# Optimization experiments

Measured on AMD Instinct MI355X. Metric: run time of the kernel, lower is better.

## Reference

```python
import jax, jax.numpy as jnp
import numpy as np

N_SPANS = 4096
EMB_DIM = 384
HEADS = 4
DECAY_LAMBDA = 5.0
THRESHOLD = 0.1
NEG_SLOPE = 0.2  # PyG GATConv default leaky_relu slope


def setup_inputs() -> dict:
    key = jax.random.key(0)
    k1, k2, k3, k4, k5, k6 = jax.random.split(key, 6)
    embeddings = jax.random.normal(k1, (N_SPANS, EMB_DIM), dtype=jnp.float32)
    span_positions = jnp.sort(
        jax.random.randint(k2, (N_SPANS, 2), 0, 100000), axis=1
    ).astype(jnp.int64)
    # GATConv params: lin (no bias), per-head attention vectors, output bias
    glorot = 1.0 / np.sqrt(EMB_DIM)
    W = jax.random.normal(k3, (EMB_DIM, HEADS, EMB_DIM), dtype=jnp.float32) * glorot
    att_src = jax.random.normal(k4, (HEADS, EMB_DIM), dtype=jnp.float32) * glorot
    att_dst = jax.random.normal(k5, (HEADS, EMB_DIM), dtype=jnp.float32) * glorot
    bias = jnp.zeros((EMB_DIM,), dtype=jnp.float32)
    return {
        "embeddings": embeddings,
        "span_positions": span_positions,
        "W": W,
        "att_src": att_src,
        "att_dst": att_dst,
        "bias": bias,
    }


def _adjacency_mask(embeddings):
    # A_ij = cos_sim(e_i, e_j) * exp(-|i - j| / lambda); edges where A > 0.1
    n = embeddings.shape[0]
    en = embeddings / jnp.linalg.norm(embeddings, axis=1, keepdims=True)
    cos_sim = en @ en.T  # [N, N]
    idx = jnp.arange(n, dtype=embeddings.dtype)
    decay = jnp.exp(-jnp.abs(idx[None, :] - idx[:, None]) / DECAY_LAMBDA)
    adj = cos_sim * decay
    # diagonal is 1.0 > threshold, so self-loops (required by GATConv) are present
    return adj > THRESHOLD  # symmetric mask: mask[i, j] == edge j -> i


def reference(embeddings, span_positions, W, att_src, att_dst, bias):
    mask = _adjacency_mask(embeddings)  # [N_dst, N_src]
    # GATConv(heads=4, concat=False): project, per-head additive attention
    x = jnp.einsum("nd,dhe->nhe", embeddings, W)  # [N, H, E]
    a_src = jnp.einsum("nhe,he->nh", x, att_src)  # [N, H]
    a_dst = jnp.einsum("nhe,he->nh", x, att_dst)  # [N, H]
    # logits[i, j, h] for edge j -> i
    logits = jax.nn.leaky_relu(a_dst[:, None, :] + a_src[None, :, :], NEG_SLOPE)
    logits = jnp.where(mask[:, :, None], logits, jnp.float32(-jnp.inf))
    alpha = jax.nn.softmax(logits, axis=1)  # softmax over incoming sources j
    out = jnp.einsum("ijh,jhe->ihe", alpha, x)  # [N, H, E]
    out = out.mean(axis=1) + bias  # concat=False -> mean over heads, then bias
    return out
```

## Files before the change

### kernel.cpp

```cpp
#include <hip/hip_runtime.h>
#include <hip/hip_bf16.h>
#include <math.h>

#define N_SPANS 4096
#define EMB 384
#define HEADS 4
#define HE (HEADS * EMB)
#define BAND 11
#define BW (2 * BAND + 1)

typedef short bf16x8 __attribute__((ext_vector_type(8)));
typedef float f32x4 __attribute__((ext_vector_type(4)));
typedef unsigned short u16x8 __attribute__((ext_vector_type(8)));

__device__ __forceinline__ unsigned short f2bf(float f) {
    union { float f; unsigned u; } x; x.f = f;
    unsigned r = x.u + 0x7fffu + ((x.u >> 16) & 1u);
    return (unsigned short)(r >> 16);
}

__device__ __forceinline__ float wave_sum(float v) {
    #pragma unroll
    for (int off = 32; off; off >>= 1) v += __shfl_xor(v, off, 64);
    return v;
}
__device__ __forceinline__ float wave_max(float v) {
    #pragma unroll
    for (int off = 32; off; off >>= 1) v = fmaxf(v, __shfl_xor(v, off, 64));
    return v;
}

__global__ __launch_bounds__(256) void row_norms(const float* __restrict__ E,
                                                 float* __restrict__ invn) {
    int n = blockIdx.x * 4 + (threadIdx.x >> 6);
    int lane = threadIdx.x & 63;
    const float* er = E + n * EMB;
    float s = 0.f;
    #pragma unroll
    for (int m = 0; m < 6; ++m) { float v = er[m * 64 + lane]; s += v * v; }
    s = wave_sum(s);
    if (lane == 0) invn[n] = 1.0f / sqrtf(s);
}

__global__ __launch_bounds__(256) void transpose_w(const float* __restrict__ W,
                                                   unsigned short* __restrict__ Wt) {
    __shared__ float t[32][33];
    int n0 = blockIdx.x * 32;
    int k0 = blockIdx.y * 32;
    int tx = threadIdx.x & 31, ty = threadIdx.x >> 5;
    #pragma unroll
    for (int q = 0; q < 4; ++q)
        t[ty + q * 8][tx] = W[(k0 + ty + q * 8) * HE + n0 + tx];
    __syncthreads();
    #pragma unroll
    for (int q = 0; q < 4; ++q)
        Wt[(n0 + ty + q * 8) * EMB + k0 + tx] = f2bf(t[tx][ty + q * 8]);
}

__global__ __launch_bounds__(256) void gemm_proj(const float* __restrict__ E,
                                                 const unsigned short* __restrict__ Wt,
                                                 float* __restrict__ X) {
    __shared__ unsigned short As[128 * 32];
    __shared__ unsigned short Bs[128 * 32];
    const int tid = threadIdx.x;
    const int lane = tid & 63;
    const int wave = tid >> 6;
    const int m0 = blockIdx.y * 128;
    const int n0 = blockIdx.x * 128;
    const int wr = (wave >> 1) * 64;
    const int wc = (wave & 1) * 64;
    const int quad = lane >> 4;
    const int l16 = lane & 15;

    f32x4 acc[4][4];
    #pragma unroll
    for (int i = 0; i < 4; ++i)
        #pragma unroll
        for (int j = 0; j < 4; ++j) acc[i][j] = 0.f;

    for (int kt = 0; kt < 12; ++kt) {
        __syncthreads();
        #pragma unroll
        for (int c = 0; c < 4; ++c) {
            int ch = tid + c * 256;
            int row = ch >> 3, cc = ch & 7;
            const float4 v = *(const float4*)(E + (m0 + row) * EMB + kt * 32 + cc * 4);
            ushort4 b;
            b.x = f2bf(v.x); b.y = f2bf(v.y); b.z = f2bf(v.z); b.w = f2bf(v.w);
            *(ushort4*)(&As[row * 32 + cc * 4]) = b;
        }
        #pragma unroll
        for (int c = 0; c < 2; ++c) {
            int ch = tid + c * 256;
            int row = ch >> 2, cc = ch & 3;
            *(u16x8*)(&Bs[row * 32 + cc * 8]) =
                *(const u16x8*)(Wt + (n0 + row) * EMB + kt * 32 + cc * 8);
        }
        __syncthreads();

        bf16x8 af[4], bfr[4];
        #pragma unroll
        for (int t = 0; t < 4; ++t) {
            af[t]  = *(const bf16x8*)(&As[(wr + t * 16 + l16) * 32 + quad * 8]);
            bfr[t] = *(const bf16x8*)(&Bs[(wc + t * 16 + l16) * 32 + quad * 8]);
        }
        #pragma unroll
        for (int ti = 0; ti < 4; ++ti)
            #pragma unroll
            for (int tj = 0; tj < 4; ++tj)
                acc[ti][tj] = __builtin_amdgcn_mfma_f32_16x16x32_bf16(
                    af[ti], bfr[tj], acc[ti][tj], 0, 0, 0);
    }
    #pragma unroll
    for (int ti = 0; ti < 4; ++ti)
        #pragma unroll
        for (int tj = 0; tj < 4; ++tj) {
            int col = n0 + wc + tj * 16 + l16;
            #pragma unroll
            for (int r = 0; r < 4; ++r) {
                int row = m0 + wr + ti * 16 + quad * 4 + r;
                X[row * HE + col] = acc[ti][tj][r];
            }
        }
}

__global__ __launch_bounds__(256) void att_vecs(const float* __restrict__ X,
                                                const float* __restrict__ att_src,
                                                const float* __restrict__ att_dst,
                                                float* __restrict__ asrc,
                                                float* __restrict__ adst) {
    int n = blockIdx.x;
    int lane = threadIdx.x & 63, h = threadIdx.x >> 6;
    const float* xr = X + n * HE + h * EMB;
    float ss = 0.f, sd = 0.f;
    #pragma unroll
    for (int m = 0; m < 6; ++m) {
        int e = m * 64 + lane;
        float v = xr[e];
        ss += v * att_src[h * EMB + e];
        sd += v * att_dst[h * EMB + e];
    }
    ss = wave_sum(ss);
    sd = wave_sum(sd);
    if (lane == 0) { asrc[n * HEADS + h] = ss; adst[n * HEADS + h] = sd; }
}

__global__ __launch_bounds__(256) void band_attn(const float* __restrict__ E,
                                                 const float* __restrict__ invn,
                                                 const float* __restrict__ asrc,
                                                 const float* __restrict__ adst,
                                                 const float* __restrict__ X,
                                                 const float* __restrict__ bias,
                                                 float* __restrict__ out) {
    const int i = blockIdx.x;
    const int tid = threadIdx.x;
    const int lane = tid & 63, wave = tid >> 6;

    __shared__ float ei[EMB];
    __shared__ float alpha_s[HEADS][BW];
    __shared__ int maskv[BW];
    __shared__ int list[BW];
    __shared__ int cnt;

    for (int d = tid; d < EMB; d += 256) ei[d] = E[i * EMB + d];
    __syncthreads();

    const float inv_i = invn[i];
    for (int it = 0; it < 6; ++it) {
        int jo = it * 4 + wave;
        if (jo < BW) {
            int j = i - BAND + jo;
            bool valid = (j >= 0) && (j < N_SPANS);
            float s = 0.f;
            if (valid) {
                const float* ej = E + j * EMB;
                #pragma unroll
                for (int m = 0; m < 6; ++m) {
                    int d = m * 64 + lane;
                    s += ei[d] * ej[d];
                }
                s = wave_sum(s);
            }
            if (lane == 0) {
                int mflag = 0;
                if (valid) {
                    float cosv = s * inv_i * invn[j];
                    int dd = jo - BAND; if (dd < 0) dd = -dd;
                    float a = cosv * expf(-(float)dd * 0.2f);
                    if (a > 0.1f) mflag = 1;
                }
                maskv[jo] = mflag;
            }
        }
    }
    __syncthreads();

    {
        const int h = wave;
        const int jo = lane;
        float logit = -INFINITY;
        if (jo < BW && maskv[jo]) {
            int j = i - BAND + jo;
            float z = adst[i * HEADS + h] + asrc[j * HEADS + h];
            logit = (z >= 0.f) ? z : 0.2f * z;
        }
        float mx = wave_max(logit);
        float ex = (jo < BW) ? expf(logit - mx) : 0.f;
        float sm = wave_sum(ex);
        if (jo < BW) alpha_s[h][jo] = ex / sm;
    }
    __syncthreads();

    if (tid == 0) {
        int c = 0;
        for (int jo = 0; jo < BW; ++jo) if (maskv[jo]) list[c++] = jo;
        cnt = c;
    }
    __syncthreads();

    const int c = cnt;
    for (int e = tid; e < EMB; e += 256) {
        float acc = 0.f;
        for (int ii = 0; ii < c; ++ii) {
            int jo = list[ii];
            int j = i - BAND + jo;
            const float* xb = X + j * HE + e;
            #pragma unroll
            for (int h = 0; h < HEADS; ++h)
                acc += alpha_s[h][jo] * xb[h * EMB];
        }
        out[i * EMB + e] = 0.25f * acc + bias[e];
    }
}

extern "C" void kernel_launch(void* const* d_in, const int* in_sizes, int n_in,
                              void* d_out, int out_size, void* d_ws, size_t ws_size,
                              hipStream_t stream) {
    const float* E       = (const float*)d_in[0];
    const float* W       = (const float*)d_in[2];
    const float* att_src = (const float*)d_in[3];
    const float* att_dst = (const float*)d_in[4];
    const float* bias    = (const float*)d_in[5];
    float* out = (float*)d_out;

    char* ws = (char*)d_ws;
    float* X            = (float*)ws;
    unsigned short* Wt  = (unsigned short*)(ws + 25165824);
    float* invn         = (float*)(ws + 25165824 + 1179648);
    float* asrc         = invn + 4096;
    float* adst         = asrc + 4096 * HEADS;

    row_norms<<<1024, 256, 0, stream>>>(E, invn);
    transpose_w<<<dim3(48, 12), 256, 0, stream>>>(W, Wt);
    gemm_proj<<<dim3(12, 32), 256, 0, stream>>>(E, Wt, X);
    att_vecs<<<4096, 256, 0, stream>>>(X, att_src, att_dst, asrc, adst);
    band_attn<<<4096, 256, 0, stream>>>(E, invn, asrc, adst, X, bias, out);
}
```

Measured before the change: 120.6 us.

## Fuse prep kernels, attention-vector reduction into GEMM epilogue, store projection in bf16

Merges row norms, the weight transpose, a pre-pass casting embeddings to bf16, and zeroing of the atomic accumulators into one prep launch. The GEMM now loads tiles with direct global-to-LDS loads and computes the per-head source/destination attention scalars in its epilogue via shuffles and atomics, which removes the separate att_vecs pass over X. X is stored as bf16, halving its write and the band_attn gather traffic. The cost is extra bf16 rounding on X, atomic ordering nondeterminism in the attention scalars, and fewer kernel launches.

Measured after the change: 119.0 us (median of 2 runs). Within noise of the previous version (-1.3%).

```diff
diff --git a/kernel.cpp b/kernel.cpp
--- a/kernel.cpp
+++ b/kernel.cpp
@@ -11,13 +11,15 @@
 
 typedef short bf16x8 __attribute__((ext_vector_type(8)));
 typedef float f32x4 __attribute__((ext_vector_type(4)));
-typedef unsigned short u16x8 __attribute__((ext_vector_type(8)));
 
 __device__ __forceinline__ unsigned short f2bf(float f) {
     union { float f; unsigned u; } x; x.f = f;
     unsigned r = x.u + 0x7fffu + ((x.u >> 16) & 1u);
     return (unsigned short)(r >> 16);
 }
+__device__ __forceinline__ float bf2f(unsigned short u) {
+    union { unsigned u; float f; } x; x.u = ((unsigned)u) << 16; return x.f;
+}
 
 __device__ __forceinline__ float wave_sum(float v) {
     #pragma unroll
@@ -30,36 +32,67 @@
     return v;
 }
 
-__global__ __launch_bounds__(256) void row_norms(const float* __restrict__ E,
-                                                 float* __restrict__ invn) {
-    int n = blockIdx.x * 4 + (threadIdx.x >> 6);
-    int lane = threadIdx.x & 63;
-    const float* er = E + n * EMB;
-    float s = 0.f;
-    #pragma unroll
-    for (int m = 0; m < 6; ++m) { float v = er[m * 64 + lane]; s += v * v; }
-    s = wave_sum(s);
-    if (lane == 0) invn[n] = 1.0f / sqrtf(s);
-}
-
-__global__ __launch_bounds__(256) void transpose_w(const float* __restrict__ W,
-                                                   unsigned short* __restrict__ Wt) {
-    __shared__ float t[32][33];
-    int n0 = blockIdx.x * 32;
-    int k0 = blockIdx.y * 32;
-    int tx = threadIdx.x & 31, ty = threadIdx.x >> 5;
-    #pragma unroll
-    for (int q = 0; q < 4; ++q)
-        t[ty + q * 8][tx] = W[(k0 + ty + q * 8) * HE + n0 + tx];
-    __syncthreads();
-    #pragma unroll
-    for (int q = 0; q < 4; ++q)
-        Wt[(n0 + ty + q * 8) * EMB + k0 + tx] = f2bf(t[tx][ty + q * 8]);
-}
-
-__global__ __launch_bounds__(256) void gemm_proj(const float* __restrict__ E,
+__device__ __forceinline__ void gl2lds16(const void* g, void* l) {
+    __builtin_amdgcn_global_load_lds(
+        (const __attribute__((address_space(1))) void*)(uintptr_t)g,
+        (__attribute__((address_space(3))) void*)(unsigned)(uintptr_t)l,
+        16, 0, 0);
+}
+
+__global__ __launch_bounds__(256) void prep(const float* __restrict__ E,
+                                            const float* __restrict__ W,
+                                            unsigned short* __restrict__ Ebf,
+                                            unsigned short* __restrict__ Wt,
+                                            float* __restrict__ invn,
+                                            float* __restrict__ attacc) {
+    __shared__ float tile[32][33];
+    const int b = blockIdx.x;
+    const int tid = threadIdx.x;
+    if (b < 1024) {
+        const int lane = tid & 63, w = tid >> 6;
+        const int n = b * 4 + w;
+        const float4* er = (const float4*)(E + n * EMB);
+        unsigned short* orow = Ebf + n * EMB;
+        float s = 0.f;
+        float4 v0 = er[lane];
+        s += v0.x * v0.x + v0.y * v0.y + v0.z * v0.z + v0.w * v0.w;
+        ushort4 c0;
+        c0.x = f2bf(v0.x); c0.y = f2bf(v0.y); c0.z = f2bf(v0.z); c0.w = f2bf(v0.w);
+        ((ushort4*)orow)[lane] = c0;
+        if (lane < 32) {
+            float4 v1 = er[lane + 64];
+            s += v1.x * v1.x + v1.y * v1.y + v1.z * v1.z + v1.w * v1.w;
+            ushort4 c1;
+            c1.x = f2bf(v1.x); c1.y = f2bf(v1.y); c1.z = f2bf(v1.z); c1.w = f2bf(v1.w);
+            ((ushort4*)orow)[lane + 64] = c1;
+        }
+        s = wave_sum(s);
+        if (lane == 0) invn[n] = 1.0f / sqrtf(s);
+    } else if (b < 1600) {
+        const int t = b - 1024;
+        const int n0 = (t % 48) * 32;
+        const int k0 = (t / 48) * 32;
+        const int tx = tid & 31, ty = tid >> 5;
+        #pragma unroll
+        for (int q = 0; q < 4; ++q)
+            tile[ty + q * 8][tx] = W[(k0 + ty + q * 8) * HE + n0 + tx];
+        __syncthreads();
+        #pragma unroll
+        for (int q = 0; q < 4; ++q)
+            Wt[(n0 + ty + q * 8) * EMB + k0 + tx] = f2bf(tile[tx][ty + q * 8]);
+    } else {
+        const int t = b - 1600;
+        ((float4*)attacc)[t * 256 + tid] = make_float4(0.f, 0.f, 0.f, 0.f);
+    }
+}
+
+__global__ __launch_bounds__(256) void gemm_attn(const unsigned short* __restrict__ Ebf,
                                                  const unsigned short* __restrict__ Wt,
-                                                 float* __restrict__ X) {
+                                                 const float* __restrict__ attS,
+                                                 const float* __restrict__ attD,
+                                                 unsigned short* __restrict__ Xb,
+                                                 float* __restrict__ asrc,
+                                                 float* __restrict__ adst) {
     __shared__ unsigned short As[128 * 32];
     __shared__ unsigned short Bs[128 * 32];
     const int tid = threadIdx.x;
@@ -72,6 +105,11 @@
     const int quad = lane >> 4;
     const int l16 = lane & 15;
 
+    const char* Ab = (const char*)Ebf + (size_t)(m0 + wave * 32 + (lane >> 2)) * 768 + (lane & 3) * 16;
+    const char* Bb = (const char*)Wt  + (size_t)(n0 + wave * 32 + (lane >> 2)) * 768 + (lane & 3) * 16;
+    char* AsB = (char*)As + wave * 32 * 64;
+    char* BsB = (char*)Bs + wave * 32 * 64;
+
     f32x4 acc[4][4];
     #pragma unroll
     for (int i = 0; i < 4; ++i)
@@ -79,23 +117,12 @@
         for (int j = 0; j < 4; ++j) acc[i][j] = 0.f;
 
     for (int kt = 0; kt < 12; ++kt) {
+        const int kb = kt * 64;
         __syncthreads();
-        #pragma unroll
-        for (int c = 0; c < 4; ++c) {
-            int ch = tid + c * 256;
-            int row = ch >> 3, cc = ch & 7;
-            const float4 v = *(const float4*)(E + (m0 + row) * EMB + kt * 32 + cc * 4);
-            ushort4 b;
-            b.x = f2bf(v.x); b.y = f2bf(v.y); b.z = f2bf(v.z); b.w = f2bf(v.w);
-            *(ushort4*)(&As[row * 32 + cc * 4]) = b;
-        }
-        #pragma unroll
-        for (int c = 0; c < 2; ++c) {
-            int ch = tid + c * 256;
-            int row = ch >> 2, cc = ch & 3;
-            *(u16x8*)(&Bs[row * 32 + cc * 8]) =
-                *(const u16x8*)(Wt + (n0 + row) * EMB + kt * 32 + cc * 8);
-        }
+        gl2lds16(Ab + kb,            AsB);
+        gl2lds16(Ab + kb + 16 * 768, AsB + 16 * 64);
+        gl2lds16(Bb + kb,            BsB);
+        gl2lds16(Bb + kb + 16 * 768, BsB + 16 * 64);
         __syncthreads();
 
         bf16x8 af[4], bfr[4];
@@ -111,6 +138,38 @@
                 acc[ti][tj] = __builtin_amdgcn_mfma_f32_16x16x32_bf16(
                     af[ti], bfr[tj], acc[ti][tj], 0, 0, 0);
     }
+
+    const int hblk = (n0 + wc) / EMB;
+    float aS[4], aD[4];
+    #pragma unroll
+    for (int tj = 0; tj < 4; ++tj) {
+        int col = n0 + wc + tj * 16 + l16;
+        aS[tj] = attS[col];
+        aD[tj] = attD[col];
+    }
+    #pragma unroll
+    for (int ti = 0; ti < 4; ++ti)
+        #pragma unroll
+        for (int r = 0; r < 4; ++r) {
+            float ps = 0.f, pd = 0.f;
+            #pragma unroll
+            for (int tj = 0; tj < 4; ++tj) {
+                float v = acc[ti][tj][r];
+                ps += v * aS[tj];
+                pd += v * aD[tj];
+            }
+            #pragma unroll
+            for (int off = 1; off < 16; off <<= 1) {
+                ps += __shfl_xor(ps, off, 64);
+                pd += __shfl_xor(pd, off, 64);
+            }
+            if (l16 == 0) {
+                int row = m0 + wr + ti * 16 + quad * 4 + r;
+                atomicAdd(&asrc[row * HEADS + hblk], ps);
+                atomicAdd(&adst[row * HEADS + hblk], pd);
+            }
+        }
+
     #pragma unroll
     for (int ti = 0; ti < 4; ++ti)
         #pragma unroll
@@ -119,37 +178,16 @@
             #pragma unroll
             for (int r = 0; r < 4; ++r) {
                 int row = m0 + wr + ti * 16 + quad * 4 + r;
-                X[row * HE + col] = acc[ti][tj][r];
-            }
-        }
-}
-
-__global__ __launch_bounds__(256) void att_vecs(const float* __restrict__ X,
-                                                const float* __restrict__ att_src,
-                                                const float* __restrict__ att_dst,
-                                                float* __restrict__ asrc,
-                                                float* __restrict__ adst) {
-    int n = blockIdx.x;
-    int lane = threadIdx.x & 63, h = threadIdx.x >> 6;
-    const float* xr = X + n * HE + h * EMB;
-    float ss = 0.f, sd = 0.f;
-    #pragma unroll
-    for (int m = 0; m < 6; ++m) {
-        int e = m * 64 + lane;
-        float v = xr[e];
-        ss += v * att_src[h * EMB + e];
-        sd += v * att_dst[h * EMB + e];
-    }
-    ss = wave_sum(ss);
-    sd = wave_sum(sd);
-    if (lane == 0) { asrc[n * HEADS + h] = ss; adst[n * HEADS + h] = sd; }
+                Xb[row * HE + col] = f2bf(acc[ti][tj][r]);
+            }
+        }
 }
 
 __global__ __launch_bounds__(256) void band_attn(const float* __restrict__ E,
                                                  const float* __restrict__ invn,
                                                  const float* __restrict__ asrc,
                                                  const float* __restrict__ adst,
-                                                 const float* __restrict__ X,
+                                                 const unsigned short* __restrict__ Xb,
                                                  const float* __restrict__ bias,
                                                  float* __restrict__ out) {
     const int i = blockIdx.x;
@@ -224,10 +262,10 @@
         for (int ii = 0; ii < c; ++ii) {
             int jo = list[ii];
             int j = i - BAND + jo;
-            const float* xb = X + j * HE + e;
+            const unsigned short* xb = Xb + j * HE + e;
             #pragma unroll
             for (int h = 0; h < HEADS; ++h)
-                acc += alpha_s[h][jo] * xb[h * EMB];
+                acc += alpha_s[h][jo] * bf2f(xb[h * EMB]);
         }
         out[i * EMB + e] = 0.25f * acc + bias[e];
     }
@@ -244,15 +282,14 @@
     float* out = (float*)d_out;
 
     char* ws = (char*)d_ws;
-    float* X            = (float*)ws;
-    unsigned short* Wt  = (unsigned short*)(ws + 25165824);
-    float* invn         = (float*)(ws + 25165824 + 1179648);
-    float* asrc         = invn + 4096;
-    float* adst         = asrc + 4096 * HEADS;
-
-    row_norms<<<1024, 256, 0, stream>>>(E, invn);
-    transpose_w<<<dim3(48, 12), 256, 0, stream>>>(W, Wt);
-    gemm_proj<<<dim3(12, 32), 256, 0, stream>>>(E, Wt, X);
-    att_vecs<<<4096, 256, 0, stream>>>(X, att_src, att_dst, asrc, adst);
-    band_attn<<<4096, 256, 0, stream>>>(E, invn, asrc, adst, X, bias, out);
-}
+    unsigned short* Xb  = (unsigned short*)ws;
+    unsigned short* Ebf = (unsigned short*)(ws + 12582912);
+    unsigned short* Wt  = (unsigned short*)(ws + 15728640);
+    float* invn         = (float*)(ws + 16908288);
+    float* asrc         = (float*)(ws + 16924672);
+    float* adst         = (float*)(ws + 16990208);
+
+    prep<<<1632, 256, 0, stream>>>(E, W, Ebf, Wt, invn, asrc );
+    gemm_attn<<<dim3(12, 32), 256, 0, stream>>>(Ebf, Wt, att_src, att_dst, Xb, asrc, adst);
+    band_attn<<<4096, 256, 0, stream>>>(E, invn, asrc, adst, Xb, bias, out);
+}
```
